# Performance work log

Measured on AMD Instinct MI355X. Metric: run time of the kernel, lower is better.

The kernel has to match this reference:

```python
import jax, jax.numpy as jnp
import numpy as np

B, C, M, N = 8, 256, 4, 2048
CK = C // M  # k_conv input channels
EPS_BN = 1e-5


def setup_inputs() -> dict:
    key = jax.random.key(0)
    ks = jax.random.split(key, 10)
    s = 0.05
    return {
        "q": jax.random.normal(ks[0], (B, C, N), jnp.float32),
        "x": jax.random.normal(ks[1], (B, CK, N), jnp.float32),
        "Wq": jax.random.normal(ks[2], (C, C), jnp.float32) * s,   # q_conv (no bias)
        "Wk": jax.random.normal(ks[3], (C, CK), jnp.float32) * s,  # k_conv (no bias)
        "Wv": jax.random.normal(ks[4], (C, C), jnp.float32) * s,   # v_conv
        "bv": jax.random.normal(ks[5], (C,), jnp.float32) * s,
        "Wt": jax.random.normal(ks[6], (C, C), jnp.float32) * s,   # trans_conv
        "bt": jax.random.normal(ks[7], (C,), jnp.float32) * s,
        "gamma": jnp.ones((C,), jnp.float32),                      # BatchNorm1d weight
        "beta": jnp.zeros((C,), jnp.float32),                      # BatchNorm1d bias
    }


def reference(q, x, Wq, Wk, Wv, bv, Wt, bt, gamma, beta):
    # 1x1 Conv1d == per-point channel matmul
    x_q = jnp.einsum("oc,bcn->bno", Wq, q)                  # [B, N, C]
    x_k = jnp.einsum("oc,bcn->bon", Wk, x)                  # [B, C, N]
    x_v = jnp.einsum("oc,bcn->bon", Wv, q) + bv[None, :, None]  # [B, C, N]

    energy = jnp.einsum("bnc,bcm->bnm", x_q, x_k)           # [B, Nq, Nk]
    attention = jax.nn.softmax(energy, axis=-1)
    # extra L1 renormalization over the query dimension (dim=1)
    attention = attention / (1e-9 + attention.sum(axis=1, keepdims=True))

    x_r = jnp.einsum("bcn,bnm->bcm", x_v, attention)        # [B, C, Nk]

    y = jnp.einsum("oc,bcn->bon", Wt, x_r) + bt[None, :, None]
    # BatchNorm1d in training mode: batch statistics over (B, N) per channel
    mean = y.mean(axis=(0, 2), keepdims=True)
    var = ((y - mean) ** 2).mean(axis=(0, 2), keepdims=True)
    y = (y - mean) * jax.lax.rsqrt(var + EPS_BN)
    y = y * gamma[None, :, None] + beta[None, :, None]
    return jax.nn.relu(y)
```

## Files before the change

### kernel.cpp

```cpp
#include <hip/hip_runtime.h>
#include <hip/hip_bf16.h>

#define NB  8
#define NC  256
#define NCK 64
#define SEQ 2048

typedef unsigned short u16;
typedef short bfrag8 __attribute__((ext_vector_type(8)));
typedef float ffrag4 __attribute__((ext_vector_type(4)));

#define MFMA16(a, b, c) __builtin_amdgcn_mfma_f32_16x16x32_bf16((a), (b), (c), 0, 0, 0)

static __device__ __forceinline__ u16 f2bf(float f) {
  return __builtin_bit_cast(u16, (__bf16)f);
}
static __device__ __forceinline__ float bf2f(u16 u) {
  unsigned v = (unsigned)u << 16;
  return __builtin_bit_cast(float, v);
}

__global__ __launch_bounds__(256) void wconv_kernel(
    const float* __restrict__ Wv, const float* __restrict__ Wt,
    u16* __restrict__ dst, float* __restrict__ zz, float* __restrict__ rowsum_g,
    const float* __restrict__ Wq, const float* __restrict__ Wk,
    u16* __restrict__ Gh, u16* __restrict__ Gl) {
  int bx = blockIdx.x;
  if (bx >= 512) {
    if (bx == 512) {
      zz[threadIdx.x] = 0.f;
      zz[256 + threadIdx.x] = 0.f;
    } else if (bx < 577) {
      rowsum_g[(bx - 513) * 256 + threadIdx.x] = 0.f;
    } else {
      const int ck = bx - 577, c = threadIdx.x;
      float s = 0.f;
#pragma unroll 8
      for (int o = 0; o < 256; ++o) s += Wq[o * 256 + c] * Wk[o * 64 + ck];
      u16 h = f2bf(s);
      Gh[ck * 256 + c] = h;
      Gl[ck * 256 + c] = f2bf(s - bf2f(h));
    }
    return;
  }
  int id = bx * 256 + threadIdx.x;
  const float* src;
  int off;
  if (id < 65536) { src = Wv; off = 131072; }
  else            { src = Wt; off = 262144; id -= 65536; }
  float v = src[id];
  u16 h = f2bf(v);
  u16 l = f2bf(v - bf2f(h));
  dst[off + id] = h;
  dst[off + 65536 + id] = l;
}

template <int CIN>
static __device__ __forceinline__ void tconv_body(
    const float* __restrict__ in, u16* __restrict__ Thi, u16* __restrict__ Tlo,
    int bxl, int by, int tid) {
  __shared__ float t[32][33];
  const int b = bxl & 7, cg = bxl >> 3;
  const int c0 = cg << 5, n0 = by << 5;
  {
    int c = tid >> 3, m4 = (tid & 7) << 2;
    float4 v = *(const float4*)&in[((size_t)b * CIN + c0 + c) * SEQ + n0 + m4];
    t[c][m4 + 0] = v.x; t[c][m4 + 1] = v.y; t[c][m4 + 2] = v.z; t[c][m4 + 3] = v.w;
  }
  __syncthreads();
  {
    int n = tid >> 3, c4 = (tid & 7) << 2;
    u16 h[4], l[4];
#pragma unroll
    for (int j = 0; j < 4; ++j) {
      float v = t[c4 + j][n];
      h[j] = f2bf(v);
      l[j] = f2bf(v - bf2f(h[j]));
    }
    size_t base = ((size_t)b * SEQ + n0 + n) * CIN + c0 + c4;
    *(uint2*)&Thi[base] = make_uint2((unsigned)h[0] | ((unsigned)h[1] << 16),
                                     (unsigned)h[2] | ((unsigned)h[3] << 16));
    *(uint2*)&Tlo[base] = make_uint2((unsigned)l[0] | ((unsigned)l[1] << 16),
                                     (unsigned)l[2] | ((unsigned)l[3] << 16));
  }
}

__global__ __launch_bounds__(256) void tconv2_kernel(
    const float* __restrict__ q, const float* __restrict__ x,
    u16* __restrict__ qTh, u16* __restrict__ qTl,
    u16* __restrict__ xTh, u16* __restrict__ xTl) {
  if (blockIdx.x < 64)
    tconv_body<NC>(q, qTh, qTl, blockIdx.x, blockIdx.y, threadIdx.x);
  else
    tconv_body<NCK>(x, xTh, xTl, blockIdx.x - 64, blockIdx.y, threadIdx.x);
}

template <int K>
__global__ __launch_bounds__(256, 2) void gemm_kernel(
    const u16* __restrict__ Ahi, const u16* __restrict__ Alo,
    const u16* __restrict__ Whi, const u16* __restrict__ Wlo,
    const float* __restrict__ bias, u16* __restrict__ outp) {
  constexpr int SP = K + 8;
  extern __shared__ u16 lds[];
  const int tid = threadIdx.x;
  const int wv = tid >> 6, lane = tid & 63, quad = lane >> 4, ln = lane & 15;
  const int b = blockIdx.x & 7, nt = blockIdx.x >> 3;
  const int o0 = blockIdx.y << 6, n0 = nt << 7;

  constexpr int RW = K / 8;
  for (int i = tid; i < 64 * RW; i += 256) {
    int row = i / RW, kc = (i % RW) * 8;
    *(uint4*)&lds[row * SP + kc] = *(const uint4*)&Whi[(size_t)(o0 + row) * K + kc];
    *(uint4*)&lds[(64 + row) * SP + kc] = *(const uint4*)&Wlo[(size_t)(o0 + row) * K + kc];
  }
  constexpr int NA = K / 32;
  bfrag8 ahi[2][NA], alo[2][NA];
#pragma unroll
  for (int rs = 0; rs < 2; ++rs) {
    const u16* ap = Ahi + ((size_t)b * SEQ + n0 + wv * 32 + rs * 16 + ln) * K + quad * 8;
    const u16* al = Alo + ((size_t)b * SEQ + n0 + wv * 32 + rs * 16 + ln) * K + quad * 8;
#pragma unroll
    for (int a = 0; a < NA; ++a) {
      ahi[rs][a] = *(const bfrag8*)(ap + a * 32);
      alo[rs][a] = *(const bfrag8*)(al + a * 32);
    }
  }
  __syncthreads();

  ffrag4 acc[2][4];
#pragma unroll
  for (int ot = 0; ot < 4; ++ot) {
    ffrag4 e0 = {0.f, 0.f, 0.f, 0.f}, e1 = {0.f, 0.f, 0.f, 0.f};
#pragma unroll
    for (int a = 0; a < NA; ++a) {
      bfrag8 wh = *(const bfrag8*)&lds[(ot * 16 + ln) * SP + a * 32 + quad * 8];
      bfrag8 wl = *(const bfrag8*)&lds[(64 + ot * 16 + ln) * SP + a * 32 + quad * 8];
      e0 = MFMA16(wh, ahi[0][a], e0);
      e0 = MFMA16(wh, alo[0][a], e0);
      e0 = MFMA16(wl, ahi[0][a], e0);
      e1 = MFMA16(wh, ahi[1][a], e1);
      e1 = MFMA16(wh, alo[1][a], e1);
      e1 = MFMA16(wl, ahi[1][a], e1);
    }
    acc[0][ot] = e0;
    acc[1][ot] = e1;
  }
  __syncthreads();

  u16* tl = lds;
#pragma unroll
  for (int rs = 0; rs < 2; ++rs)
#pragma unroll
    for (int ot = 0; ot < 4; ++ot)
#pragma unroll
      for (int r = 0; r < 4; ++r)
        tl[(ot * 16 + quad * 4 + r) * 136 + wv * 32 + rs * 16 + ln] = f2bf(acc[rs][ot][r]);
  __syncthreads();
  for (int i = tid; i < 64 * 16; i += 256) {
    int row = i >> 4, n8 = (i & 15) * 8;
    float bb = (bias != nullptr) ? bias[o0 + row] : 0.f;
    u16 pk[8];
#pragma unroll
    for (int j = 0; j < 8; ++j) pk[j] = f2bf(bf2f(tl[row * 136 + n8 + j]) + bb);
    int t = (n0 + n8) >> 5, no = n8 & 31;
    *(uint4*)&outp[(((size_t)b * 64 + t) * NC + o0 + row) * 32 + no] = *(uint4*)pk;
  }
}

__global__ __launch_bounds__(256, 2) void gemmxg_kernel(
    const u16* __restrict__ Ahi, const u16* __restrict__ Alo,
    const u16* __restrict__ Gh, const u16* __restrict__ Gl,
    u16* __restrict__ xg) {
  constexpr int K = 256, SP = K + 8;
  __shared__ u16 lds[128 * SP];
  const int tid = threadIdx.x;
  const int wv = tid >> 6, lane = tid & 63, quad = lane >> 4, ln = lane & 15;
  const int b = blockIdx.x & 7, nt = blockIdx.x >> 3;
  const int n0 = nt << 7;

  for (int i = tid; i < 64 * 32; i += 256) {
    int row = i >> 5, kc = (i & 31) * 8;
    *(uint4*)&lds[row * SP + kc] = *(const uint4*)&Gh[(size_t)row * K + kc];
    *(uint4*)&lds[(64 + row) * SP + kc] = *(const uint4*)&Gl[(size_t)row * K + kc];
  }
  bfrag8 ahi[2][8], alo[2][8];
#pragma unroll
  for (int rs = 0; rs < 2; ++rs) {
    const u16* ap = Ahi + ((size_t)b * SEQ + n0 + wv * 32 + rs * 16 + ln) * K + quad * 8;
    const u16* al = Alo + ((size_t)b * SEQ + n0 + wv * 32 + rs * 16 + ln) * K + quad * 8;
#pragma unroll
    for (int a = 0; a < 8; ++a) {
      ahi[rs][a] = *(const bfrag8*)(ap + a * 32);
      alo[rs][a] = *(const bfrag8*)(al + a * 32);
    }
  }
  __syncthreads();

  ffrag4 acc[2][4];
#pragma unroll
  for (int ot = 0; ot < 4; ++ot) {
    ffrag4 e0 = {0.f, 0.f, 0.f, 0.f}, e1 = {0.f, 0.f, 0.f, 0.f};
#pragma unroll
    for (int a = 0; a < 8; ++a) {
      bfrag8 wh = *(const bfrag8*)&lds[(ot * 16 + ln) * SP + a * 32 + quad * 8];
      bfrag8 wl = *(const bfrag8*)&lds[(64 + ot * 16 + ln) * SP + a * 32 + quad * 8];
      e0 = MFMA16(ahi[0][a], wh, e0);
      e0 = MFMA16(alo[0][a], wh, e0);
      e0 = MFMA16(ahi[0][a], wl, e0);
      e1 = MFMA16(ahi[1][a], wh, e1);
      e1 = MFMA16(alo[1][a], wh, e1);
      e1 = MFMA16(ahi[1][a], wl, e1);
    }
    acc[0][ot] = e0;
    acc[1][ot] = e1;
  }
  __syncthreads();

  u16* tl = lds;
#pragma unroll
  for (int rs = 0; rs < 2; ++rs)
#pragma unroll
    for (int ot = 0; ot < 4; ++ot)
#pragma unroll
      for (int r = 0; r < 4; ++r)
        tl[(wv * 32 + rs * 16 + quad * 4 + r) * 72 + ot * 16 + ln] = f2bf(acc[rs][ot][r]);
  __syncthreads();
  for (int i = tid; i < 128 * 8; i += 256) {
    int row = i >> 3, c8 = (i & 7) * 8;
    *(uint4*)&xg[((size_t)b * SEQ + n0 + row) * NCK + c8] = *(uint4*)&tl[row * 72 + c8];
  }
}

__global__ __launch_bounds__(256, 2) void rowsum_kernel(
    const u16* __restrict__ xg, const u16* __restrict__ xTh,
    const u16* __restrict__ xTl, float* __restrict__ rowsum_g) {
  __shared__ u16 bk_l[2][2][64 * 76];
  const int tid = threadIdx.x;
  const int wv = tid >> 6, lane = tid & 63, quad = lane >> 4, ln = lane & 15;
  const int b  = blockIdx.x & 7;
  const int nt = (blockIdx.x >> 3) & 15;
  const int mh = blockIdx.x >> 7;
  const int n0 = nt << 7;
  const int m0 = mh << 9;

  bfrag8 aq[2][2];
#pragma unroll
  for (int rs = 0; rs < 2; ++rs) {
    const u16* qp = xg + ((size_t)b * SEQ + n0 + wv * 32 + rs * 16 + ln) * NCK + quad * 8;
    aq[rs][0] = *(const bfrag8*)qp;
    aq[rs][1] = *(const bfrag8*)(qp + 32);
  }

  const int srow = tid >> 2, scol = (tid & 3) << 4;
  uint4 ph0, ph1, pl0, pl1;
  {
    size_t base = ((size_t)b * SEQ + m0 + srow) * NCK + scol;
    ph0 = *(const uint4*)&xTh[base];     ph1 = *(const uint4*)&xTh[base + 8];
    pl0 = *(const uint4*)&xTl[base];     pl1 = *(const uint4*)&xTl[base + 8];
  }

  float rsum[2][4];
#pragma unroll
  for (int rs = 0; rs < 2; ++rs)
#pragma unroll
    for (int r = 0; r < 4; ++r) rsum[rs][r] = 0.f;

  for (int ch = 0; ch < 8; ++ch) {
    u16* bh = &bk_l[ch & 1][0][srow * 76 + scol];
    u16* bl = &bk_l[ch & 1][1][srow * 76 + scol];
    *(uint4*)bh = ph0; *(uint4*)(bh + 8) = ph1;
    *(uint4*)bl = pl0; *(uint4*)(bl + 8) = pl1;
    if (ch < 7) {
      size_t base = ((size_t)b * SEQ + m0 + (ch + 1) * 64 + srow) * NCK + scol;
      ph0 = *(const uint4*)&xTh[base];   ph1 = *(const uint4*)&xTh[base + 8];
      pl0 = *(const uint4*)&xTl[base];   pl1 = *(const uint4*)&xTl[base + 8];
    }
    __syncthreads();

    ffrag4 e[2][4];
#pragma unroll
    for (int rs = 0; rs < 2; ++rs)
#pragma unroll
      for (int ms = 0; ms < 4; ++ms) e[rs][ms] = (ffrag4){0.f, 0.f, 0.f, 0.f};
#pragma unroll
    for (int ms = 0; ms < 4; ++ms)
#pragma unroll
      for (int kk = 0; kk < 2; ++kk) {
        bfrag8 bbh = *(const bfrag8*)&bk_l[ch & 1][0][(ms * 16 + ln) * 76 + kk * 32 + quad * 8];
        bfrag8 bbl = *(const bfrag8*)&bk_l[ch & 1][1][(ms * 16 + ln) * 76 + kk * 32 + quad * 8];
        e[0][ms] = MFMA16(aq[0][kk], bbh, e[0][ms]);
        e[0][ms] = MFMA16(aq[0][kk], bbl, e[0][ms]);
        e[1][ms] = MFMA16(aq[1][kk], bbh, e[1][ms]);
        e[1][ms] = MFMA16(aq[1][kk], bbl, e[1][ms]);
      }
#pragma unroll
    for (int rs = 0; rs < 2; ++rs)
#pragma unroll
      for (int ms = 0; ms < 4; ++ms)
#pragma unroll
        for (int r = 0; r < 4; ++r) rsum[rs][r] += __expf(e[rs][ms][r]);
  }

#pragma unroll
  for (int msk = 1; msk < 16; msk <<= 1)
#pragma unroll
    for (int rs = 0; rs < 2; ++rs)
#pragma unroll
      for (int r = 0; r < 4; ++r) rsum[rs][r] += __shfl_xor(rsum[rs][r], msk, 64);
  if (ln == 0) {
#pragma unroll
    for (int rs = 0; rs < 2; ++rs)
#pragma unroll
      for (int r = 0; r < 4; ++r)
        atomicAdd(&rowsum_g[(size_t)b * SEQ + n0 + wv * 32 + rs * 16 + quad * 4 + r],
                  rsum[rs][r]);
  }
}

__global__ __launch_bounds__(512, 4) void attn_kernel(
    const u16* __restrict__ xg, const u16* __restrict__ xTh,
    const u16* __restrict__ xTl, const u16* __restrict__ xv,
    const float* __restrict__ rowsum_g,
    u16* __restrict__ U, float* __restrict__ csum) {
  __shared__ u16 xg_l[32 * 76];
  __shared__ u16 p_l[64 * 40];
  __shared__ float ri_l[1024];
  __shared__ float cs_l[64];
  const int tid = threadIdx.x;
  const int wv = tid >> 6, lane = tid & 63, quad = lane >> 4, ln = lane & 15;
  const int b = blockIdx.x & 7;
  const int m0 = ((blockIdx.x >> 3) & 31) << 6;
  const int half = blockIdx.x >> 8;
  const int nsub = wv & 1, msub = wv >> 1;
  const int nt0 = half * 32, ntEnd = nt0 + 32;

  if (tid < 64) cs_l[tid] = 0.f;
  {
    const float* rp = &rowsum_g[(size_t)b * SEQ + (half << 10)];
    ri_l[tid] = 1.0f / rp[tid];
    ri_l[tid + 512] = 1.0f / rp[tid + 512];
  }

  bfrag8 bkh[2], bkl[2];
  {
    size_t base = ((size_t)b * SEQ + m0 + msub * 16 + ln) * NCK + quad * 8;
#pragma unroll
    for (int kk = 0; kk < 2; ++kk) {
      bkh[kk] = *(const bfrag8*)&xTh[base + kk * 32];
      bkl[kk] = *(const bfrag8*)&xTl[base + kk * 32];
    }
  }

  const int prow = (tid & 255) >> 3, pcol = (tid & 7) << 3;
  uint4 pf0 = {0, 0, 0, 0};
  bfrag8 avpf0, avpf1;
  {
    if (tid < 256)
      pf0 = *(const uint4*)&xg[((size_t)b * SEQ + (nt0 << 5) + prow) * NCK + pcol];
    const u16* vp = &xv[(((size_t)b * 64 + nt0) * NC + wv * 32 + ln) * 32 + quad * 8];
    avpf0 = *(const bfrag8*)vp;
    avpf1 = *(const bfrag8*)(vp + 512);
  }

  ffrag4 acc[2][4];
#pragma unroll
  for (int ct = 0; ct < 2; ++ct)
#pragma unroll
    for (int s = 0; s < 4; ++s) acc[ct][s] = (ffrag4){0.f, 0.f, 0.f, 0.f};
  float cs = 0.f;

  for (int nt = nt0; nt < ntEnd; ++nt) {
    bfrag8 av0 = avpf0, av1 = avpf1;
    if (tid < 256) *(uint4*)&xg_l[prow * 76 + pcol] = pf0;
    {
      const int ntn = (nt + 1 < ntEnd) ? nt + 1 : nt;
      if (tid < 256)
        pf0 = *(const uint4*)&xg[((size_t)b * SEQ + (ntn << 5) + prow) * NCK + pcol];
      const u16* vp = &xv[(((size_t)b * 64 + ntn) * NC + wv * 32 + ln) * 32 + quad * 8];
      avpf0 = *(const bfrag8*)vp;
      avpf1 = *(const bfrag8*)(vp + 512);
    }
    __syncthreads();
    {
      ffrag4 e = {0.f, 0.f, 0.f, 0.f};
#pragma unroll
      for (int kk = 0; kk < 2; ++kk) {
        bfrag8 a = *(const bfrag8*)&xg_l[(nsub * 16 + ln) * 76 + kk * 32 + quad * 8];
        e = MFMA16(a, bkh[kk], e);
        e = MFMA16(a, bkl[kk], e);
      }
      const float* rp = &ri_l[((nt - nt0) << 5) + nsub * 16 + quad * 4];
      float4 ri4 = *(const float4*)rp;
      float rr[4] = {ri4.x, ri4.y, ri4.z, ri4.w};
      u16 pu[4];
#pragma unroll
      for (int r = 0; r < 4; ++r) {
        float p = __expf(e[r]) * rr[r];
        cs += p;
        pu[r] = f2bf(p);
      }
      *(uint2*)&p_l[(msub * 16 + ln) * 40 + nsub * 16 + quad * 4] =
          make_uint2((unsigned)pu[0] | ((unsigned)pu[1] << 16),
                     (unsigned)pu[2] | ((unsigned)pu[3] << 16));
    }
    __syncthreads();
#pragma unroll
    for (int s = 0; s < 4; ++s) {
      bfrag8 pb = *(const bfrag8*)&p_l[(s * 16 + ln) * 40 + quad * 8];
      acc[0][s] = MFMA16(av0, pb, acc[0][s]);
      acc[1][s] = MFMA16(av1, pb, acc[1][s]);
    }
  }

  cs += __shfl_down(cs, 32, 64);
  cs += __shfl_down(cs, 16, 64);
  if (lane < 16) atomicAdd(&cs_l[msub * 16 + ln], cs);
  __syncthreads();
  if (tid < 64) csum[((size_t)half * NB + b) * SEQ + m0 + tid] = cs_l[tid];

  u16* Uh = U + (size_t)half * NB * SEQ * NC;
#pragma unroll
  for (int ct = 0; ct < 2; ++ct)
#pragma unroll
    for (int s = 0; s < 4; ++s) {
      u16 pk[4];
#pragma unroll
      for (int r = 0; r < 4; ++r) pk[r] = f2bf(acc[ct][s][r]);
      *(uint2*)&Uh[((size_t)b * SEQ + m0 + s * 16 + ln) * NC + wv * 32 + ct * 16 + quad * 4] =
          make_uint2((unsigned)pk[0] | ((unsigned)pk[1] << 16),
                     (unsigned)pk[2] | ((unsigned)pk[3] << 16));
    }
}

__global__ __launch_bounds__(256, 2) void gemmt_kernel(
    const u16* __restrict__ U, const float* __restrict__ csum,
    const u16* __restrict__ Whi, const u16* __restrict__ Wlo,
    const float* __restrict__ bias, float* __restrict__ outp,
    float* __restrict__ ssum, float* __restrict__ sqsum) {
  constexpr int K = NC, SP = K + 8;
  __shared__ u16 lds[128 * SP];
  __shared__ float bsum[64], bsq[64];
  const int tid = threadIdx.x;
  const int wv = tid >> 6, lane = tid & 63, quad = lane >> 4, ln = lane & 15;
  const int b = blockIdx.x & 7, nt = blockIdx.x >> 3;
  const int o0 = blockIdx.y << 6, n0 = nt << 7;
  const size_t SZu = (size_t)NB * SEQ * NC;

  if (tid < 64) { bsum[tid] = 0.f; bsq[tid] = 0.f; }

  for (int i = tid; i < 64 * 32; i += 256) {
    int row = i >> 5, kc = (i & 31) * 8;
    *(uint4*)&lds[row * SP + kc] = *(const uint4*)&Whi[(size_t)(o0 + row) * K + kc];
    *(uint4*)&lds[(64 + row) * SP + kc] = *(const uint4*)&Wlo[(size_t)(o0 + row) * K + kc];
  }

  bfrag8 af[2][8];
#pragma unroll
  for (int rs = 0; rs < 2; ++rs) {
    const int row = n0 + wv * 32 + rs * 16 + ln;
    const float ic = 1.0f / (1e-9f + csum[(size_t)b * SEQ + row] +
                             csum[((size_t)NB + b) * SEQ + row]);
    const u16* up = U + ((size_t)b * SEQ + row) * NC + quad * 8;
#pragma unroll
    for (int a = 0; a < 8; ++a) {
      bfrag8 u0 = *(const bfrag8*)(up + a * 32);
      bfrag8 u1 = *(const bfrag8*)(up + SZu + a * 32);
      union { u16 u[8]; bfrag8 f; } t;
#pragma unroll
      for (int j = 0; j < 8; ++j)
        t.u[j] = f2bf((bf2f((u16)u0[j]) + bf2f((u16)u1[j])) * ic);
      af[rs][a] = t.f;
    }
  }
  __syncthreads();

  ffrag4 acc[2][4];
#pragma unroll
  for (int ot = 0; ot < 4; ++ot) {
    ffrag4 e0 = {0.f, 0.f, 0.f, 0.f}, e1 = {0.f, 0.f, 0.f, 0.f};
#pragma unroll
    for (int a = 0; a < 8; ++a) {
      bfrag8 wh = *(const bfrag8*)&lds[(ot * 16 + ln) * SP + a * 32 + quad * 8];
      bfrag8 wl = *(const bfrag8*)&lds[(64 + ot * 16 + ln) * SP + a * 32 + quad * 8];
      e0 = MFMA16(wh, af[0][a], e0);
      e0 = MFMA16(wl, af[0][a], e0);
      e1 = MFMA16(wh, af[1][a], e1);
      e1 = MFMA16(wl, af[1][a], e1);
    }
    acc[0][ot] = e0;
    acc[1][ot] = e1;
  }
  __syncthreads();

  float* fl = (float*)lds;
#pragma unroll
  for (int rs = 0; rs < 2; ++rs)
#pragma unroll
    for (int ot = 0; ot < 4; ++ot)
#pragma unroll
      for (int r = 0; r < 4; ++r)
        fl[(ot * 16 + quad * 4 + r) * 132 + wv * 32 + rs * 16 + ln] = acc[rs][ot][r];
  __syncthreads();
  for (int i = tid; i < 64 * 32; i += 256) {
    int row = i >> 5, n4 = (i & 31) * 4;
    float bb = (bias != nullptr) ? bias[o0 + row] : 0.f;
    const float* src = &fl[row * 132 + n4];
    float4 v = *(const float4*)src;
    v.x += bb; v.y += bb; v.z += bb; v.w += bb;
    *(float4*)&outp[((size_t)b * NC + o0 + row) * SEQ + n0 + n4] = v;
    float s = v.x + v.y + v.z + v.w;
    float sq = v.x * v.x + v.y * v.y + v.z * v.z + v.w * v.w;
    atomicAdd(&bsum[row], s);
    atomicAdd(&bsq[row], sq);
  }
  __syncthreads();
  if (tid < 64) {
    atomicAdd(&ssum[o0 + tid], bsum[tid]);
    atomicAdd(&sqsum[o0 + tid], bsq[tid]);
  }
}

__global__ __launch_bounds__(256) void bnorm_kernel(
    const float* __restrict__ y, const float* __restrict__ ssum, const float* __restrict__ sqsum,
    const float* __restrict__ gamma, const float* __restrict__ beta, float* __restrict__ out) {
  size_t e0 = ((size_t)blockIdx.x * 256 + threadIdx.x) * 4;
  int o = (int)((e0 >> 11) & (NC - 1));
  const float invn = 1.0f / 16384.0f;
  float mean = ssum[o] * invn;
  float var = sqsum[o] * invn - mean * mean;
  float rs = rsqrtf(var + 1e-5f);
  float a = gamma[o] * rs;
  float c = beta[o] - mean * a;
  float4 v = *(const float4*)(y + e0);
  float4 r;
  r.x = fmaxf(0.f, fmaf(v.x, a, c));
  r.y = fmaxf(0.f, fmaf(v.y, a, c));
  r.z = fmaxf(0.f, fmaf(v.z, a, c));
  r.w = fmaxf(0.f, fmaf(v.w, a, c));
  *(float4*)(out + e0) = r;
}

extern "C" void kernel_launch(void* const* d_in, const int* in_sizes, int n_in,
                              void* d_out, int out_size, void* d_ws, size_t ws_size,
                              hipStream_t stream) {
  const float* q     = (const float*)d_in[0];
  const float* x     = (const float*)d_in[1];
  const float* Wq    = (const float*)d_in[2];
  const float* Wk    = (const float*)d_in[3];
  const float* Wv    = (const float*)d_in[4];
  const float* bv    = (const float*)d_in[5];
  const float* Wt    = (const float*)d_in[6];
  const float* bt    = (const float*)d_in[7];
  const float* gamma = (const float*)d_in[8];
  const float* beta  = (const float*)d_in[9];
  float* out = (float*)d_out;

  const size_t SZ = (size_t)NB * NC * SEQ;
  const size_t SZB = SZ * 4;
  char* wsb = (char*)d_ws;
  u16* qT_hi = (u16*)(wsb);
  u16* qT_lo = qT_hi + SZ;
  u16* Ua    = (u16*)(wsb);
  float* y   = (float*)(wsb + 2 * SZB);
  u16* xv    = (u16*)(wsb + 3 * SZB);
  u16* wpack = (u16*)(wsb + 3 * SZB + SZB / 2);
  u16* Wv_hi = wpack + 131072, *Wv_lo = wpack + 196608;
  u16* Wt_hi = wpack + 262144, *Wt_lo = wpack + 327680;
  float* rowsum_g = (float*)(wpack + 425984);
  float* csum = rowsum_g + (size_t)NB * SEQ;
  float* ssum = csum + 2 * (size_t)NB * SEQ;
  float* sqsum = ssum + NC;
  u16* xT_hi = (u16*)(wsb + ((size_t)64 << 20));
  u16* xT_lo = (u16*)(wsb + ((size_t)66 << 20));
  u16* xg    = (u16*)(wsb + ((size_t)72 << 20));
  u16* Gp_hi = (u16*)(wsb + ((size_t)78 << 20));
  u16* Gp_lo = Gp_hi + 64 * 256;

  wconv_kernel<<<641, 256, 0, stream>>>(Wv, Wt, wpack, ssum, rowsum_g,
                                        Wq, Wk, Gp_hi, Gp_lo);
  tconv2_kernel<<<dim3(80, 64), 256, 0, stream>>>(q, x, qT_hi, qT_lo, xT_hi, xT_lo);

  const size_t shm256 = 64 * (256 + 8) * 2 * sizeof(u16);
  gemm_kernel<256><<<dim3(128, 4), 256, shm256, stream>>>(
      qT_hi, qT_lo, Wv_hi, Wv_lo, bv, xv);
  gemmxg_kernel<<<128, 256, 0, stream>>>(qT_hi, qT_lo, Gp_hi, Gp_lo, xg);

  rowsum_kernel<<<512, 256, 0, stream>>>(xg, xT_hi, xT_lo, rowsum_g);
  attn_kernel<<<512, 512, 0, stream>>>(xg, xT_hi, xT_lo, xv, rowsum_g, Ua, csum);
  gemmt_kernel<<<dim3(128, 4), 256, 0, stream>>>(
      Ua, csum, Wt_hi, Wt_lo, bt, y, ssum, sqsum);

  bnorm_kernel<<<4096, 256, 0, stream>>>(y, ssum, sqsum, gamma, beta, out);
}
```

Baseline: 209.2 us.

## Retile attention kernel to 256-thread blocks over 32 key columns

The attention kernel now uses 256-thread blocks, each covering 32 key positions instead of 64, launched as 1024 blocks instead of 512. Each wave now computes 64 output channels across 2 column subtiles instead of 32 channels across 4. All threads take part in the xg tile load instead of half of them. This gives more, smaller blocks for scheduling, but the energy/exp work per key column is recomputed twice as often across blocks (4 waves per 32 columns vs 8 per 64), and each wave holds more V fragments in registers.

```diff
diff --git a/kernel.cpp b/kernel.cpp
--- a/kernel.cpp
+++ b/kernel.cpp
@@ -317,28 +317,30 @@
   }
 }
 
-__global__ __launch_bounds__(512, 4) void attn_kernel(
+__global__ __launch_bounds__(256, 4) void attn_kernel(
     const u16* __restrict__ xg, const u16* __restrict__ xTh,
     const u16* __restrict__ xTl, const u16* __restrict__ xv,
     const float* __restrict__ rowsum_g,
     u16* __restrict__ U, float* __restrict__ csum) {
   __shared__ u16 xg_l[32 * 76];
-  __shared__ u16 p_l[64 * 40];
+  __shared__ u16 p_l[32 * 40];
   __shared__ float ri_l[1024];
-  __shared__ float cs_l[64];
+  __shared__ float cs_l[32];
   const int tid = threadIdx.x;
   const int wv = tid >> 6, lane = tid & 63, quad = lane >> 4, ln = lane & 15;
   const int b = blockIdx.x & 7;
-  const int m0 = ((blockIdx.x >> 3) & 31) << 6;
-  const int half = blockIdx.x >> 8;
+  const int m0 = ((blockIdx.x >> 3) & 63) << 5;
+  const int half = blockIdx.x >> 9;
   const int nsub = wv & 1, msub = wv >> 1;
   const int nt0 = half * 32, ntEnd = nt0 + 32;
 
-  if (tid < 64) cs_l[tid] = 0.f;
+  if (tid < 32) cs_l[tid] = 0.f;
   {
     const float* rp = &rowsum_g[(size_t)b * SEQ + (half << 10)];
     ri_l[tid] = 1.0f / rp[tid];
+    ri_l[tid + 256] = 1.0f / rp[tid + 256];
     ri_l[tid + 512] = 1.0f / rp[tid + 512];
+    ri_l[tid + 768] = 1.0f / rp[tid + 768];
   }
 
   bfrag8 bkh[2], bkl[2];
@@ -351,44 +353,46 @@
     }
   }
 
-  const int prow = (tid & 255) >> 3, pcol = (tid & 7) << 3;
-  uint4 pf0 = {0, 0, 0, 0};
-  bfrag8 avpf0, avpf1;
+  const int prow = tid >> 3, pcol = (tid & 7) << 3;
+  uint4 pf0;
+  bfrag8 avpf[4];
   {
-    if (tid < 256)
-      pf0 = *(const uint4*)&xg[((size_t)b * SEQ + (nt0 << 5) + prow) * NCK + pcol];
-    const u16* vp = &xv[(((size_t)b * 64 + nt0) * NC + wv * 32 + ln) * 32 + quad * 8];
-    avpf0 = *(const bfrag8*)vp;
-    avpf1 = *(const bfrag8*)(vp + 512);
-  }
-
-  ffrag4 acc[2][4];
-#pragma unroll
-  for (int ct = 0; ct < 2; ++ct)
-#pragma unroll
-    for (int s = 0; s < 4; ++s) acc[ct][s] = (ffrag4){0.f, 0.f, 0.f, 0.f};
+    pf0 = *(const uint4*)&xg[((size_t)b * SEQ + (nt0 << 5) + prow) * NCK + pcol];
+#pragma unroll
+    for (int ct = 0; ct < 4; ++ct)
+      avpf[ct] = *(const bfrag8*)&xv[(((size_t)b * 64 + nt0) * NC +
+                                      wv * 64 + ct * 16 + ln) * 32 + quad * 8];
+  }
+
+  ffrag4 acc[4][2];
+#pragma unroll
+  for (int ct = 0; ct < 4; ++ct)
+#pragma unroll
+    for (int s = 0; s < 2; ++s) acc[ct][s] = (ffrag4){0.f, 0.f, 0.f, 0.f};
   float cs = 0.f;
 
   for (int nt = nt0; nt < ntEnd; ++nt) {
-    bfrag8 av0 = avpf0, av1 = avpf1;
-    if (tid < 256) *(uint4*)&xg_l[prow * 76 + pcol] = pf0;
+    bfrag8 av[4];
+#pragma unroll
+    for (int ct = 0; ct < 4; ++ct) av[ct] = avpf[ct];
+    *(uint4*)&xg_l[prow * 76 + pcol] = pf0;
     {
       const int ntn = (nt + 1 < ntEnd) ? nt + 1 : nt;
-      if (tid < 256)
-        pf0 = *(const uint4*)&xg[((size_t)b * SEQ + (ntn << 5) + prow) * NCK + pcol];
-      const u16* vp = &xv[(((size_t)b * 64 + ntn) * NC + wv * 32 + ln) * 32 + quad * 8];
-      avpf0 = *(const bfrag8*)vp;
-      avpf1 = *(const bfrag8*)(vp + 512);
+      pf0 = *(const uint4*)&xg[((size_t)b * SEQ + (ntn << 5) + prow) * NCK + pcol];
+#pragma unroll
+      for (int ct = 0; ct < 4; ++ct)
+        avpf[ct] = *(const bfrag8*)&xv[(((size_t)b * 64 + ntn) * NC +
+                                        wv * 64 + ct * 16 + ln) * 32 + quad * 8];
     }
     __syncthreads();
     {
       ffrag4 e = {0.f, 0.f, 0.f, 0.f};
-#pragma unroll
-      for (int kk = 0; kk < 2; ++kk) {
-        bfrag8 a = *(const bfrag8*)&xg_l[(nsub * 16 + ln) * 76 + kk * 32 + quad * 8];
-        e = MFMA16(a, bkh[kk], e);
-        e = MFMA16(a, bkl[kk], e);
-      }
+      bfrag8 a0 = *(const bfrag8*)&xg_l[(nsub * 16 + ln) * 76 + quad * 8];
+      bfrag8 a1 = *(const bfrag8*)&xg_l[(nsub * 16 + ln) * 76 + 32 + quad * 8];
+      e = MFMA16(a0, bkh[0], e);
+      e = MFMA16(a0, bkl[0], e);
+      e = MFMA16(a1, bkh[1], e);
+      e = MFMA16(a1, bkl[1], e);
       const float* rp = &ri_l[((nt - nt0) << 5) + nsub * 16 + quad * 4];
       float4 ri4 = *(const float4*)rp;
       float rr[4] = {ri4.x, ri4.y, ri4.z, ri4.w};
@@ -405,10 +409,11 @@
     }
     __syncthreads();
 #pragma unroll
-    for (int s = 0; s < 4; ++s) {
+    for (int s = 0; s < 2; ++s) {
       bfrag8 pb = *(const bfrag8*)&p_l[(s * 16 + ln) * 40 + quad * 8];
-      acc[0][s] = MFMA16(av0, pb, acc[0][s]);
-      acc[1][s] = MFMA16(av1, pb, acc[1][s]);
+#pragma unroll
+      for (int ct = 0; ct < 4; ++ct)
+        acc[ct][s] = MFMA16(av[ct], pb, acc[ct][s]);
     }
   }
 
@@ -416,17 +421,17 @@
   cs += __shfl_down(cs, 16, 64);
   if (lane < 16) atomicAdd(&cs_l[msub * 16 + ln], cs);
   __syncthreads();
-  if (tid < 64) csum[((size_t)half * NB + b) * SEQ + m0 + tid] = cs_l[tid];
+  if (tid < 32) csum[((size_t)half * NB + b) * SEQ + m0 + tid] = cs_l[tid];
 
   u16* Uh = U + (size_t)half * NB * SEQ * NC;
 #pragma unroll
-  for (int ct = 0; ct < 2; ++ct)
-#pragma unroll
-    for (int s = 0; s < 4; ++s) {
+  for (int ct = 0; ct < 4; ++ct)
+#pragma unroll
+    for (int s = 0; s < 2; ++s) {
       u16 pk[4];
 #pragma unroll
       for (int r = 0; r < 4; ++r) pk[r] = f2bf(acc[ct][s][r]);
-      *(uint2*)&Uh[((size_t)b * SEQ + m0 + s * 16 + ln) * NC + wv * 32 + ct * 16 + quad * 4] =
+      *(uint2*)&Uh[((size_t)b * SEQ + m0 + s * 16 + ln) * NC + wv * 64 + ct * 16 + quad * 4] =
           make_uint2((unsigned)pk[0] | ((unsigned)pk[1] << 16),
                      (unsigned)pk[2] | ((unsigned)pk[3] << 16));
     }
@@ -586,7 +591,7 @@
   gemmxg_kernel<<<128, 256, 0, stream>>>(qT_hi, qT_lo, Gp_hi, Gp_lo, xg);
 
   rowsum_kernel<<<512, 256, 0, stream>>>(xg, xT_hi, xT_lo, rowsum_g);
-  attn_kernel<<<512, 512, 0, stream>>>(xg, xT_hi, xT_lo, xv, rowsum_g, Ua, csum);
+  attn_kernel<<<1024, 256, 0, stream>>>(xg, xT_hi, xT_lo, xv, rowsum_g, Ua, csum);
   gemmt_kernel<<<dim3(128, 4), 256, 0, stream>>>(
       Ua, csum, Wt_hi, Wt_lo, bt, y, ssum, sqsum);
 
```

Measured after the change: 222.7 us. 6.4% more time.

## Double-buffer LDS and software-pipeline attention loop to one barrier per tile

Applied to the files above, without the earlier changes.

Splits the xg and P shared-memory tiles into two buffers and skews the loop so the energy/softmax stage for tile t runs alongside the P·V MFMAs for tile t-1. This cuts the barriers per iteration from two to one and lets the exp work overlap with the matrix accumulation. The cost is extra LDS, more live registers for the lagged V fragments, and an epilogue step that drains the last tile.

```diff
diff --git a/kernel.cpp b/kernel.cpp
--- a/kernel.cpp
+++ b/kernel.cpp
@@ -322,8 +322,8 @@
     const u16* __restrict__ xTl, const u16* __restrict__ xv,
     const float* __restrict__ rowsum_g,
     u16* __restrict__ U, float* __restrict__ csum) {
-  __shared__ u16 xg_l[32 * 76];
-  __shared__ u16 p_l[64 * 40];
+  __shared__ u16 xg_l[2][32 * 76];
+  __shared__ u16 p_l[2][64 * 40];
   __shared__ float ri_l[1024];
   __shared__ float cs_l[64];
   const int tid = threadIdx.x;
@@ -332,7 +332,7 @@
   const int m0 = ((blockIdx.x >> 3) & 31) << 6;
   const int half = blockIdx.x >> 8;
   const int nsub = wv & 1, msub = wv >> 1;
-  const int nt0 = half * 32, ntEnd = nt0 + 32;
+  const int nt0 = half * 32;
 
   if (tid < 64) cs_l[tid] = 0.f;
   {
@@ -352,14 +352,18 @@
   }
 
   const int prow = (tid & 255) >> 3, pcol = (tid & 7) << 3;
-  uint4 pf0 = {0, 0, 0, 0};
-  bfrag8 avpf0, avpf1;
+
+  uint4 pfXg = {0, 0, 0, 0};
+  if (tid < 256) {
+    pfXg = *(const uint4*)&xg[((size_t)b * SEQ + (nt0 << 5) + prow) * NCK + pcol];
+    *(uint4*)&xg_l[0][prow * 76 + pcol] = pfXg;
+    pfXg = *(const uint4*)&xg[((size_t)b * SEQ + ((nt0 + 1) << 5) + prow) * NCK + pcol];
+  }
+  bfrag8 avP0, avP1, avC0, avC1;
   {
-    if (tid < 256)
-      pf0 = *(const uint4*)&xg[((size_t)b * SEQ + (nt0 << 5) + prow) * NCK + pcol];
     const u16* vp = &xv[(((size_t)b * 64 + nt0) * NC + wv * 32 + ln) * 32 + quad * 8];
-    avpf0 = *(const bfrag8*)vp;
-    avpf1 = *(const bfrag8*)(vp + 512);
+    avC0 = *(const bfrag8*)vp;
+    avC1 = *(const bfrag8*)(vp + 512);
   }
 
   ffrag4 acc[2][4];
@@ -369,28 +373,19 @@
     for (int s = 0; s < 4; ++s) acc[ct][s] = (ffrag4){0.f, 0.f, 0.f, 0.f};
   float cs = 0.f;
 
-  for (int nt = nt0; nt < ntEnd; ++nt) {
-    bfrag8 av0 = avpf0, av1 = avpf1;
-    if (tid < 256) *(uint4*)&xg_l[prow * 76 + pcol] = pf0;
-    {
-      const int ntn = (nt + 1 < ntEnd) ? nt + 1 : nt;
-      if (tid < 256)
-        pf0 = *(const uint4*)&xg[((size_t)b * SEQ + (ntn << 5) + prow) * NCK + pcol];
-      const u16* vp = &xv[(((size_t)b * 64 + ntn) * NC + wv * 32 + ln) * 32 + quad * 8];
-      avpf0 = *(const bfrag8*)vp;
-      avpf1 = *(const bfrag8*)(vp + 512);
-    }
-    __syncthreads();
+  __syncthreads();
+
+  for (int t = 0; t < 32; ++t) {
+    const int cur = t & 1, alt = cur ^ 1;
     {
       ffrag4 e = {0.f, 0.f, 0.f, 0.f};
-#pragma unroll
-      for (int kk = 0; kk < 2; ++kk) {
-        bfrag8 a = *(const bfrag8*)&xg_l[(nsub * 16 + ln) * 76 + kk * 32 + quad * 8];
-        e = MFMA16(a, bkh[kk], e);
-        e = MFMA16(a, bkl[kk], e);
-      }
-      const float* rp = &ri_l[((nt - nt0) << 5) + nsub * 16 + quad * 4];
-      float4 ri4 = *(const float4*)rp;
+      bfrag8 a0 = *(const bfrag8*)&xg_l[cur][(nsub * 16 + ln) * 76 + quad * 8];
+      bfrag8 a1 = *(const bfrag8*)&xg_l[cur][(nsub * 16 + ln) * 76 + 32 + quad * 8];
+      e = MFMA16(a0, bkh[0], e);
+      e = MFMA16(a0, bkl[0], e);
+      e = MFMA16(a1, bkh[1], e);
+      e = MFMA16(a1, bkl[1], e);
+      float4 ri4 = *(const float4*)&ri_l[(t << 5) + nsub * 16 + quad * 4];
       float rr[4] = {ri4.x, ri4.y, ri4.z, ri4.w};
       u16 pu[4];
 #pragma unroll
@@ -399,17 +394,38 @@
         cs += p;
         pu[r] = f2bf(p);
       }
-      *(uint2*)&p_l[(msub * 16 + ln) * 40 + nsub * 16 + quad * 4] =
+      *(uint2*)&p_l[cur][(msub * 16 + ln) * 40 + nsub * 16 + quad * 4] =
           make_uint2((unsigned)pu[0] | ((unsigned)pu[1] << 16),
                      (unsigned)pu[2] | ((unsigned)pu[3] << 16));
     }
+    if (tid < 256) *(uint4*)&xg_l[alt][prow * 76 + pcol] = pfXg;
+    bfrag8 avN0, avN1;
+    {
+      const int t2 = (t + 2 < 32) ? t + 2 : 31;
+      if (tid < 256)
+        pfXg = *(const uint4*)&xg[((size_t)b * SEQ + ((nt0 + t2) << 5) + prow) * NCK + pcol];
+      const int t1 = (t + 1 < 32) ? t + 1 : 31;
+      const u16* vp = &xv[(((size_t)b * 64 + nt0 + t1) * NC + wv * 32 + ln) * 32 + quad * 8];
+      avN0 = *(const bfrag8*)vp;
+      avN1 = *(const bfrag8*)(vp + 512);
+    }
+    if (t > 0) {
+#pragma unroll
+      for (int s = 0; s < 4; ++s) {
+        bfrag8 pb = *(const bfrag8*)&p_l[alt][(s * 16 + ln) * 40 + quad * 8];
+        acc[0][s] = MFMA16(avP0, pb, acc[0][s]);
+        acc[1][s] = MFMA16(avP1, pb, acc[1][s]);
+      }
+    }
+    avP0 = avC0; avP1 = avC1;
+    avC0 = avN0; avC1 = avN1;
     __syncthreads();
-#pragma unroll
-    for (int s = 0; s < 4; ++s) {
-      bfrag8 pb = *(const bfrag8*)&p_l[(s * 16 + ln) * 40 + quad * 8];
-      acc[0][s] = MFMA16(av0, pb, acc[0][s]);
-      acc[1][s] = MFMA16(av1, pb, acc[1][s]);
-    }
+  }
+#pragma unroll
+  for (int s = 0; s < 4; ++s) {
+    bfrag8 pb = *(const bfrag8*)&p_l[1][(s * 16 + ln) * 40 + quad * 8];
+    acc[0][s] = MFMA16(avP0, pb, acc[0][s]);
+    acc[1][s] = MFMA16(avP1, pb, acc[1][s]);
   }
 
   cs += __shfl_down(cs, 32, 64);
```

Result: no change. 210.2 us (+0.5%).

## Fuse trans-conv GEMM with BatchNorm via cooperative grid sync

Applied to the files above, without the earlier changes.

Merges the trans_conv GEMM and the BatchNorm+ReLU pass into one cooperative kernel. The biased GEMM tile stays in LDS while a grid-wide sync waits for the per-channel sums, then each block normalizes and writes the final output directly. This drops the write and re-read of the intermediate y tensor and one kernel launch. In exchange all 512 blocks must be co-resident and pay for a grid barrier; if the cooperative launch fails, the code falls back to the old two-kernel path.

```diff
diff --git a/kernel.cpp b/kernel.cpp
--- a/kernel.cpp
+++ b/kernel.cpp
@@ -1,5 +1,6 @@
 #include <hip/hip_runtime.h>
 #include <hip/hip_bf16.h>
+#include <hip/hip_cooperative_groups.h>
 
 #define NB  8
 #define NC  256
@@ -432,18 +433,15 @@
     }
 }
 
-__global__ __launch_bounds__(256, 2) void gemmt_kernel(
+static __device__ __forceinline__ void gemmt_body(
     const u16* __restrict__ U, const float* __restrict__ csum,
     const u16* __restrict__ Whi, const u16* __restrict__ Wlo,
-    const float* __restrict__ bias, float* __restrict__ outp,
-    float* __restrict__ ssum, float* __restrict__ sqsum) {
+    const float* __restrict__ bias,
+    float* __restrict__ ssum, float* __restrict__ sqsum,
+    u16* lds, float* bsum, float* bsq,
+    int tid, int b, int nt, int o0, int n0) {
   constexpr int K = NC, SP = K + 8;
-  __shared__ u16 lds[128 * SP];
-  __shared__ float bsum[64], bsq[64];
-  const int tid = threadIdx.x;
   const int wv = tid >> 6, lane = tid & 63, quad = lane >> 4, ln = lane & 15;
-  const int b = blockIdx.x & 7, nt = blockIdx.x >> 3;
-  const int o0 = blockIdx.y << 6, n0 = nt << 7;
   const size_t SZu = (size_t)NB * SEQ * NC;
 
   if (tid < 64) { bsum[tid] = 0.f; bsq[tid] = 0.f; }
@@ -504,10 +502,10 @@
   for (int i = tid; i < 64 * 32; i += 256) {
     int row = i >> 5, n4 = (i & 31) * 4;
     float bb = (bias != nullptr) ? bias[o0 + row] : 0.f;
-    const float* src = &fl[row * 132 + n4];
-    float4 v = *(const float4*)src;
+    float* src = &fl[row * 132 + n4];
+    float4 v = *(float4*)src;
     v.x += bb; v.y += bb; v.z += bb; v.w += bb;
-    *(float4*)&outp[((size_t)b * NC + o0 + row) * SEQ + n0 + n4] = v;
+    *(float4*)src = v;
     float s = v.x + v.y + v.z + v.w;
     float sq = v.x * v.x + v.y * v.y + v.z * v.z + v.w * v.w;
     atomicAdd(&bsum[row], s);
@@ -517,6 +515,65 @@
   if (tid < 64) {
     atomicAdd(&ssum[o0 + tid], bsum[tid]);
     atomicAdd(&sqsum[o0 + tid], bsq[tid]);
+  }
+}
+
+__global__ __launch_bounds__(256, 2) void gemmtbn_kernel(
+    const u16* __restrict__ U, const float* __restrict__ csum,
+    const u16* __restrict__ Whi, const u16* __restrict__ Wlo,
+    const float* __restrict__ bias, float* __restrict__ outp,
+    float* __restrict__ ssum, float* __restrict__ sqsum,
+    const float* __restrict__ gamma, const float* __restrict__ beta) {
+  constexpr int SP = NC + 8;
+  __shared__ u16 lds[128 * SP];
+  __shared__ float bsum[64], bsq[64];
+  const int tid = threadIdx.x;
+  const int b = blockIdx.x & 7, nt = blockIdx.x >> 3;
+  const int o0 = blockIdx.y << 6, n0 = nt << 7;
+
+  gemmt_body(U, csum, Whi, Wlo, bias, ssum, sqsum, lds, bsum, bsq, tid, b, nt, o0, n0);
+
+  cooperative_groups::this_grid().sync();
+
+  const float invn = 1.0f / 16384.0f;
+  float* fl = (float*)lds;
+  for (int i = tid; i < 64 * 32; i += 256) {
+    int row = i >> 5, n4 = (i & 31) * 4;
+    int o = o0 + row;
+    float mean = ssum[o] * invn;
+    float var = sqsum[o] * invn - mean * mean;
+    float rs = rsqrtf(var + 1e-5f);
+    float a = gamma[o] * rs;
+    float c = beta[o] - mean * a;
+    float4 v = *(const float4*)&fl[row * 132 + n4];
+    float4 r;
+    r.x = fmaxf(0.f, fmaf(v.x, a, c));
+    r.y = fmaxf(0.f, fmaf(v.y, a, c));
+    r.z = fmaxf(0.f, fmaf(v.z, a, c));
+    r.w = fmaxf(0.f, fmaf(v.w, a, c));
+    *(float4*)&outp[((size_t)b * NC + o) * SEQ + n0 + n4] = r;
+  }
+}
+
+__global__ __launch_bounds__(256, 2) void gemmt_kernel(
+    const u16* __restrict__ U, const float* __restrict__ csum,
+    const u16* __restrict__ Whi, const u16* __restrict__ Wlo,
+    const float* __restrict__ bias, float* __restrict__ outp,
+    float* __restrict__ ssum, float* __restrict__ sqsum) {
+  constexpr int SP = NC + 8;
+  __shared__ u16 lds[128 * SP];
+  __shared__ float bsum[64], bsq[64];
+  const int tid = threadIdx.x;
+  const int b = blockIdx.x & 7, nt = blockIdx.x >> 3;
+  const int o0 = blockIdx.y << 6, n0 = nt << 7;
+
+  gemmt_body(U, csum, Whi, Wlo, bias, ssum, sqsum, lds, bsum, bsq, tid, b, nt, o0, n0);
+
+  float* fl = (float*)lds;
+  for (int i = tid; i < 64 * 32; i += 256) {
+    int row = i >> 5, n4 = (i & 31) * 4;
+    *(float4*)&outp[((size_t)b * NC + o0 + row) * SEQ + n0 + n4] =
+        *(const float4*)&fl[row * 132 + n4];
   }
 }
 
@@ -587,8 +644,21 @@
 
   rowsum_kernel<<<512, 256, 0, stream>>>(xg, xT_hi, xT_lo, rowsum_g);
   attn_kernel<<<512, 512, 0, stream>>>(xg, xT_hi, xT_lo, xv, rowsum_g, Ua, csum);
-  gemmt_kernel<<<dim3(128, 4), 256, 0, stream>>>(
-      Ua, csum, Wt_hi, Wt_lo, bt, y, ssum, sqsum);
-
-  bnorm_kernel<<<4096, 256, 0, stream>>>(y, ssum, sqsum, gamma, beta, out);
-}
+
+  {
+    const u16* Uc = Ua;
+    const float* cc = csum;
+    const u16* Whc = Wt_hi;
+    const u16* Wlc = Wt_lo;
+    void* args[] = {(void*)&Uc, (void*)&cc, (void*)&Whc, (void*)&Wlc,
+                    (void*)&bt, (void*)&out, (void*)&ssum, (void*)&sqsum,
+                    (void*)&gamma, (void*)&beta};
+    hipError_t cerr = hipLaunchCooperativeKernel(
+        (const void*)gemmtbn_kernel, dim3(128, 4), dim3(256), args, 0, stream);
+    if (cerr != hipSuccess) {
+      gemmt_kernel<<<dim3(128, 4), 256, 0, stream>>>(
+          Ua, csum, Wt_hi, Wt_lo, bt, y, ssum, sqsum);
+      bnorm_kernel<<<4096, 256, 0, stream>>>(y, ssum, sqsum, gamma, beta, out);
+    }
+  }
+}
```

After: 267.3 us. 1.28x slower.
